# Performance work log

Hardware: AMD Instinct MI355X
Metric: run time of the kernel (lower is better)

The kernel has to match this reference:

```python
import jax, jax.numpy as jnp
import numpy as np

H, C = 5, 12            # heads, head_size
N_NODES, N_EDGES = 100000, 1600000
F_NODE, F_EDGE = 128, 32
HID, N_CLASSES = 16, 2


def _lin_init(key, din, dout, bias=True):
    k1, k2 = jax.random.split(key)
    s = 1.0 / np.sqrt(din)
    W = jax.random.uniform(k1, (din, dout), minval=-s, maxval=s, dtype=jnp.float32)
    if bias:
        b = jax.random.uniform(k2, (dout,), minval=-s, maxval=s, dtype=jnp.float32)
        return W, b
    return W


def setup_inputs() -> dict:
    key = jax.random.key(0)
    ks = jax.random.split(key, 8)
    d = {}
    d["x"] = jax.random.normal(ks[0], (N_NODES, F_NODE), dtype=jnp.float32)
    d["edge_index"] = jax.random.randint(ks[1], (2, N_EDGES), 0, N_NODES)
    d["edge_attr"] = jax.random.normal(ks[2], (N_EDGES, F_EDGE), dtype=jnp.float32)
    HC = H * C
    for i, din in [(1, F_NODE), (2, HC)]:
        kk = jax.random.split(ks[2 + i], 5)
        d[f"Wq{i}"], d[f"bq{i}"] = _lin_init(kk[0], din, HC)
        d[f"Wk{i}"], d[f"bk{i}"] = _lin_init(kk[1], din, HC)
        d[f"Wv{i}"], d[f"bv{i}"] = _lin_init(kk[2], din, HC)
        d[f"We{i}"] = _lin_init(kk[3], F_EDGE, HC, bias=False)  # lin_edge has no bias in PyG
        d[f"Ws{i}"], d[f"bs{i}"] = _lin_init(kk[4], din, HC)    # root/skip linear
    d["W1"], d["b1"] = _lin_init(ks[6], HC, HID)
    d["W2"], d["b2"] = _lin_init(ks[7], HID, N_CLASSES)
    return d


def _transformer_conv(x, src, dst, edge_attr, Wq, bq, Wk, bk, Wv, bv, We, Ws, bs):
    # PyG TransformerConv, concat=True, root_weight=True, beta=False, dropout=0
    N = x.shape[0]
    q = (x @ Wq + bq).reshape(N, H, C)
    k = (x @ Wk + bk).reshape(N, H, C)
    v = (x @ Wv + bv).reshape(N, H, C)
    e = (edge_attr @ We).reshape(-1, H, C)          # [E,H,C]
    kj = k[src] + e                                  # per-edge key
    vj = v[src] + e                                  # per-edge value
    alpha = jnp.einsum('ehc,ehc->eh', q[dst], kj) / jnp.sqrt(jnp.asarray(C, x.dtype))
    # segment-softmax over incoming edges of each destination node
    amax = jax.ops.segment_max(alpha, dst, num_segments=N)          # [N,H]
    w = jnp.exp(alpha - amax[dst])
    denom = jax.ops.segment_sum(w, dst, num_segments=N)             # [N,H]
    w = w / (denom[dst] + 1e-16)
    out = jax.ops.segment_sum(vj * w[:, :, None], dst, num_segments=N).reshape(N, H * C)
    return out + x @ Ws + bs                                         # skip/root connection


def reference(x, edge_index, edge_attr,
              Wq1, bq1, Wk1, bk1, Wv1, bv1, We1, Ws1, bs1,
              Wq2, bq2, Wk2, bk2, Wv2, bv2, We2, Ws2, bs2,
              W1, b1, W2, b2):
    src, dst = edge_index[0], edge_index[1]
    h = jax.nn.relu(_transformer_conv(x, src, dst, edge_attr, Wq1, bq1, Wk1, bk1, Wv1, bv1, We1, Ws1, bs1))
    h = jax.nn.relu(_transformer_conv(h, src, dst, edge_attr, Wq2, bq2, Wk2, bk2, Wv2, bv2, We2, Ws2, bs2))
    h = jax.nn.relu(h @ W1 + b1)
    return h @ W2 + b2
```

## Files before the change

kernel.cpp:

```cpp
#include <hip/hip_runtime.h>
#include <cstddef>

#define NN 100000
#define NE 1600000
#define NH 5
#define NC 12
#define HC 60
#define FN 128
#define FE 32
#define HID 16
#define NCLS 2

template<int DIN>
__global__ __launch_bounds__(256) void qkvs_kernel(
    const float* __restrict__ X,
    const float* __restrict__ Wq, const float* __restrict__ bq,
    const float* __restrict__ Wk, const float* __restrict__ bk,
    const float* __restrict__ Wv, const float* __restrict__ bv,
    const float* __restrict__ Ws, const float* __restrict__ bs,
    float* __restrict__ q, float* __restrict__ k,
    float* __restrict__ v, float* __restrict__ s)
{
    constexpr int NB = 8;
    const int n0 = blockIdx.x * NB;
    const int j = threadIdx.x;
    if (j >= 240) return;
    const int mat = j / 60, col = j - mat * 60;
    const float* W; const float* b; float* out;
    switch (mat) {
        case 0:  W = Wq; b = bq; out = q; break;
        case 1:  W = Wk; b = bk; out = k; break;
        case 2:  W = Wv; b = bv; out = v; break;
        default: W = Ws; b = bs; out = s; break;
    }
    const float* __restrict__ xr = X + (size_t)n0 * DIN;
    float acc[NB];
    #pragma unroll
    for (int m = 0; m < NB; ++m) acc[m] = 0.f;
    #pragma unroll 4
    for (int r = 0; r < DIN; ++r) {
        const float w = W[r * 60 + col];
        #pragma unroll
        for (int m = 0; m < NB; ++m)
            acc[m] = fmaf(xr[(size_t)m * DIN + r], w, acc[m]);
    }
    const float bb = b[col];
    #pragma unroll
    for (int m = 0; m < NB; ++m)
        out[(size_t)(n0 + m) * 60 + col] = acc[m] + bb;
}

__global__ __launch_bounds__(256) void hist_kernel(
    const int* __restrict__ ei, int* __restrict__ cnt)
{
    const int e = blockIdx.x * 256 + threadIdx.x;
    if (e < NE) atomicAdd(&cnt[ei[NE + e]], 1);
}

__global__ __launch_bounds__(1024) void scan1_kernel(
    const int* __restrict__ cnt, int* __restrict__ excl, int* __restrict__ bsum)
{
    __shared__ int sh[1024];
    const int i = blockIdx.x * 1024 + threadIdx.x;
    const int v = (i < NN) ? cnt[i] : 0;
    sh[threadIdx.x] = v;
    __syncthreads();
    for (int off = 1; off < 1024; off <<= 1) {
        const int t = (threadIdx.x >= off) ? sh[threadIdx.x - off] : 0;
        __syncthreads();
        sh[threadIdx.x] += t;
        __syncthreads();
    }
    if (i < NN) excl[i] = sh[threadIdx.x] - v;
    if (threadIdx.x == 1023) bsum[blockIdx.x] = sh[1023];
}

__global__ void scan2_kernel(int* __restrict__ bsum, int nb, int* __restrict__ start)
{
    if (threadIdx.x == 0 && blockIdx.x == 0) {
        int acc = 0;
        for (int b = 0; b < nb; ++b) { const int t = bsum[b]; bsum[b] = acc; acc += t; }
        start[NN] = acc;
    }
}

__global__ __launch_bounds__(1024) void scan3_kernel(
    int* __restrict__ start, const int* __restrict__ bsum)
{
    const int i = blockIdx.x * 1024 + threadIdx.x;
    if (i < NN) start[i] += bsum[blockIdx.x];
}

__global__ __launch_bounds__(256) void scatter_kernel(
    const int* __restrict__ ei, int* __restrict__ cursor,
    int* __restrict__ perm, int* __restrict__ srcs)
{
    const int e = blockIdx.x * 256 + threadIdx.x;
    if (e >= NE) return;
    const int d = ei[NE + e];
    const int pos = atomicAdd(&cursor[d], 1);
    perm[pos] = e;
    srcs[pos] = ei[e];
}

__global__ __launch_bounds__(256) void permea_kernel(
    const int* __restrict__ perm, const float* __restrict__ ea,
    float* __restrict__ eaP)
{
    const int t = blockIdx.x * 256 + threadIdx.x;
    const int slot = t >> 3, r4 = t & 7;
    const int e = perm[slot];
    const float4 val = ((const float4*)(ea + (size_t)e * FE))[r4];
    ((float4*)(eaP + (size_t)slot * FE))[r4] = val;
}

template<bool LIN>
__global__ __launch_bounds__(256) void agg_kernel(
    const int* __restrict__ perm, const int* __restrict__ srcs,
    const int* __restrict__ start,
    const float* __restrict__ ea, const float* __restrict__ We,
    const float* __restrict__ q, const float* __restrict__ k,
    const float* __restrict__ v, const float* __restrict__ sk,
    float* __restrict__ hout)
{
    const int wv    = threadIdx.x >> 6;
    const int lane  = threadIdx.x & 63;
    const int n     = blockIdx.x * 4 + wv;
    const int hc    = (lane < 60) ? lane : 0;
    const int hd    = hc / NC;
    const int hbase = hd * NC;
    const int c     = hc - hbase;

    const int r1 = hbase + ((c + 6) % 12);
    const int r2 = hbase + ((c + 3) % 12);
    const int r3 = hbase + ((c + 1) % 3);
    const int r4 = hbase + ((c + 2) % 3);

    float Wcol[FE];
    #pragma unroll
    for (int r = 0; r < FE; ++r) Wcol[r] = We[r * 60 + hc];

    const float qv = q[(size_t)n * 60 + hc];
    const float sv = sk[(size_t)n * 60 + hc];

    const int s0 = __builtin_amdgcn_readfirstlane(start[n]);
    const int s1 = __builtin_amdgcn_readfirstlane(start[n + 1]);

    float acc = 0.f, den = 0.f;

    auto compute = [&](const float (&EA)[FE], float KV, float VV) {
        float e0 = 0.f, e1 = 0.f;
        #pragma unroll
        for (int r = 0; r < FE; r += 2) {
            e0 = fmaf(EA[r],     Wcol[r],     e0);
            e1 = fmaf(EA[r + 1], Wcol[r + 1], e1);
        }
        const float eacc = e0 + e1;
        const float p  = qv * (KV + eacc);
        const float f1 = p  + __shfl(p,  r1);
        const float f2 = f1 + __shfl(f1, r2);
        const float a  = f2 + __shfl(f2, r3) + __shfl(f2, r4);
        const float w  = __expf(fmaf(a, 0.28867513459481287f, -20.0f));
        acc = fmaf(w, VV + eacc, acc);
        den += w;
    };

    for (int c0 = s0; c0 < s1; c0 += 64) {
        const int cnt = min(64, s1 - c0);

        int myE = 0, myS = 0;
        if (c0 + lane < s1) {
            myS = srcs[c0 + lane];
            if (!LIN) myE = perm[c0 + lane];
        }

        float eaA[FE], eaB[FE];
        float kA = 0.f, vA = 0.f, kB = 0.f, vB = 0.f;
        float kC = 0.f, vC = 0.f, kD = 0.f, vD = 0.f;

        {
            const int sA = __builtin_amdgcn_readlane(myS, 0);
            kA = k[(size_t)sA * 60 + hc];
            vA = v[(size_t)sA * 60 + hc];
            if (cnt > 1) {
                const int sB = __builtin_amdgcn_readlane(myS, 1);
                kB = k[(size_t)sB * 60 + hc];
                vB = v[(size_t)sB * 60 + hc];
            }
            const float* __restrict__ er = LIN
                ? (ea + (size_t)c0 * FE)
                : (ea + (size_t)__builtin_amdgcn_readlane(myE, 0) * FE);
            #pragma unroll
            for (int r = 0; r < FE; ++r) eaA[r] = er[r];
        }

        for (int t = 0; t < cnt; t += 2) {
            if (t + 1 < cnt) {
                const float* __restrict__ er = LIN
                    ? (ea + (size_t)(c0 + t + 1) * FE)
                    : (ea + (size_t)__builtin_amdgcn_readlane(myE, t + 1) * FE);
                #pragma unroll
                for (int r = 0; r < FE; ++r) eaB[r] = er[r];
            }
            if (t + 2 < cnt) {
                const int sC = __builtin_amdgcn_readlane(myS, t + 2);
                kC = k[(size_t)sC * 60 + hc];
                vC = v[(size_t)sC * 60 + hc];
            }
            compute(eaA, kA, vA);
            if (t + 2 < cnt) {
                const float* __restrict__ er = LIN
                    ? (ea + (size_t)(c0 + t + 2) * FE)
                    : (ea + (size_t)__builtin_amdgcn_readlane(myE, t + 2) * FE);
                #pragma unroll
                for (int r = 0; r < FE; ++r) eaA[r] = er[r];
            }
            if (t + 3 < cnt) {
                const int sD = __builtin_amdgcn_readlane(myS, t + 3);
                kD = k[(size_t)sD * 60 + hc];
                vD = v[(size_t)sD * 60 + hc];
            }
            if (t + 1 < cnt) compute(eaB, kB, vB);
            kA = kC; vA = vC; kB = kD; vB = vD;
        }
    }

    if (lane < 60)
        hout[(size_t)n * 60 + hc] = fmaxf(acc / (den + 1e-16f) + sv, 0.f);
}

__global__ __launch_bounds__(256) void mlp_kernel(
    const float* __restrict__ h,
    const float* __restrict__ W1, const float* __restrict__ b1,
    const float* __restrict__ W2, const float* __restrict__ b2,
    float* __restrict__ out)
{
    __shared__ float sW1[60 * HID];
    __shared__ float sb1[HID];
    __shared__ float sW2[HID * NCLS];
    __shared__ float sb2[NCLS];
    for (int i = threadIdx.x; i < 60 * HID; i += 256) sW1[i] = W1[i];
    if (threadIdx.x < HID)        sb1[threadIdx.x] = b1[threadIdx.x];
    if (threadIdx.x < HID * NCLS) sW2[threadIdx.x] = W2[threadIdx.x];
    if (threadIdx.x < NCLS)       sb2[threadIdx.x] = b2[threadIdx.x];
    __syncthreads();

    const int n = blockIdx.x * 256 + threadIdx.x;
    if (n >= NN) return;
    const float* __restrict__ hr = h + (size_t)n * 60;
    float hv[60];
    #pragma unroll
    for (int i = 0; i < 15; ++i) {
        const float4 t = ((const float4*)hr)[i];
        hv[4 * i + 0] = t.x; hv[4 * i + 1] = t.y;
        hv[4 * i + 2] = t.z; hv[4 * i + 3] = t.w;
    }
    float o0 = sb2[0], o1 = sb2[1];
    for (int j = 0; j < HID; ++j) {
        float t = sb1[j];
        #pragma unroll
        for (int i = 0; i < 60; ++i) t = fmaf(hv[i], sW1[i * HID + j], t);
        t = fmaxf(t, 0.f);
        o0 = fmaf(t, sW2[2 * j + 0], o0);
        o1 = fmaf(t, sW2[2 * j + 1], o1);
    }
    out[(size_t)n * 2 + 0] = o0;
    out[(size_t)n * 2 + 1] = o1;
}

extern "C" void kernel_launch(void* const* d_in, const int* in_sizes, int n_in,
                              void* d_out, int out_size, void* d_ws, size_t ws_size,
                              hipStream_t stream)
{
    const float* x   = (const float*)d_in[0];
    const int*   ei  = (const int*)  d_in[1];
    const float* ea  = (const float*)d_in[2];
    const float* Wq1 = (const float*)d_in[3];  const float* bq1 = (const float*)d_in[4];
    const float* Wk1 = (const float*)d_in[5];  const float* bk1 = (const float*)d_in[6];
    const float* Wv1 = (const float*)d_in[7];  const float* bv1 = (const float*)d_in[8];
    const float* We1 = (const float*)d_in[9];
    const float* Ws1 = (const float*)d_in[10]; const float* bs1 = (const float*)d_in[11];
    const float* Wq2 = (const float*)d_in[12]; const float* bq2 = (const float*)d_in[13];
    const float* Wk2 = (const float*)d_in[14]; const float* bk2 = (const float*)d_in[15];
    const float* Wv2 = (const float*)d_in[16]; const float* bv2 = (const float*)d_in[17];
    const float* We2 = (const float*)d_in[18];
    const float* Ws2 = (const float*)d_in[19]; const float* bs2 = (const float*)d_in[20];
    const float* W1  = (const float*)d_in[21]; const float* b1  = (const float*)d_in[22];
    const float* W2  = (const float*)d_in[23]; const float* b2  = (const float*)d_in[24];
    float* out = (float*)d_out;

    int* cnt    = (int*)d_ws;
    int* startp = cnt + NN;
    int* cursor = startp + NN + 1;
    int* bsum   = cursor + NN;
    int* perm   = bsum + 128;
    int* srcs   = perm + NE;
    const size_t int_bytes = (size_t)(3 * NN + 1 + 128 + 2 * NE) * sizeof(int);
    const size_t f_off = (int_bytes + 255) & ~(size_t)255;
    const size_t NHC = (size_t)NN * 60;
    float* qb = (float*)((char*)d_ws + f_off);
    float* kb = qb + NHC;
    float* vb = kb + NHC;
    float* sb = vb + NHC;
    float* h0 = sb + NHC;
    float* eaP = h0 + NHC;
    const size_t need = f_off + 5 * NHC * sizeof(float) + (size_t)NE * FE * sizeof(float);
    const bool lin = ws_size >= need;

    const int qkvs_blocks = NN / 8;
    const int e256_blocks = NE / 256;
    const int scan_blocks = (NN + 1023) / 1024;
    const int agg_blocks  = NN / 4;
    const int mlp_blocks  = (NN + 255) / 256;
    const int perm_blocks = NE * 8 / 256;

    hipMemsetAsync(cnt, 0, (size_t)NN * sizeof(int), stream);
    hist_kernel<<<e256_blocks, 256, 0, stream>>>(ei, cnt);
    scan1_kernel<<<scan_blocks, 1024, 0, stream>>>(cnt, startp, bsum);
    scan2_kernel<<<1, 64, 0, stream>>>(bsum, scan_blocks, startp);
    scan3_kernel<<<scan_blocks, 1024, 0, stream>>>(startp, bsum);
    hipMemcpyAsync(cursor, startp, (size_t)NN * sizeof(int),
                   hipMemcpyDeviceToDevice, stream);
    scatter_kernel<<<e256_blocks, 256, 0, stream>>>(ei, cursor, perm, srcs);
    if (lin)
        permea_kernel<<<perm_blocks, 256, 0, stream>>>(perm, ea, eaP);

    qkvs_kernel<FN><<<qkvs_blocks, 256, 0, stream>>>(
        x, Wq1, bq1, Wk1, bk1, Wv1, bv1, Ws1, bs1, qb, kb, vb, sb);
    if (lin)
        agg_kernel<true><<<agg_blocks, 256, 0, stream>>>(
            perm, srcs, startp, eaP, We1, qb, kb, vb, sb, h0);
    else
        agg_kernel<false><<<agg_blocks, 256, 0, stream>>>(
            perm, srcs, startp, ea, We1, qb, kb, vb, sb, h0);

    qkvs_kernel<HC><<<qkvs_blocks, 256, 0, stream>>>(
        h0, Wq2, bq2, Wk2, bk2, Wv2, bv2, Ws2, bs2, qb, kb, vb, sb);
    if (lin)
        agg_kernel<true><<<agg_blocks, 256, 0, stream>>>(
            perm, srcs, startp, eaP, We2, qb, kb, vb, sb, h0);
    else
        agg_kernel<false><<<agg_blocks, 256, 0, stream>>>(
            perm, srcs, startp, ea, We2, qb, kb, vb, sb, h0);

    mlp_kernel<<<mlp_blocks, 256, 0, stream>>>(h0, W1, b1, W2, b2, out);
}
```

Before: 1.264 ms.

## Fuse edge-attr permutation into scatter, retile QKVS, interleave K/V, streamline aggregation

Several changes land together. The edge-attribute permutation kernel is folded into the scatter kernel, which now copies rows with nontemporal loads and stores. The QKVS projection stages inputs in shared memory and computes 4x4 output tiles with float4 weights, writing K and V interleaved into one buffer. The single-thread block-sum scan becomes a parallel shared-memory scan. The aggregation kernel reads K/V from the interleaved layout, uses ds_bpermute for head reductions and exp2 instead of exp, and drops the per-64-edge chunking in favour of direct per-edge index loads. The goal is fewer launches and less memory traffic; the cost is more code complexity and possibly more register and LDS pressure.

New measurement: 2.295 ms. 1.82x slower.

```diff
diff --git a/kernel.cpp b/kernel.cpp
--- a/kernel.cpp
+++ b/kernel.cpp
@@ -11,6 +11,18 @@
 #define HID 16
 #define NCLS 2
 
+typedef float v4f __attribute__((ext_vector_type(4)));
+
+#if __has_builtin(__builtin_amdgcn_exp2f)
+#define EXP2F(x) __builtin_amdgcn_exp2f(x)
+#else
+#define EXP2F(x) exp2f(x)
+#endif
+
+__device__ __forceinline__ float bperm(int idxb, float x) {
+    return __int_as_float(__builtin_amdgcn_ds_bpermute(idxb, __float_as_int(x)));
+}
+
 template<int DIN>
 __global__ __launch_bounds__(256) void qkvs_kernel(
     const float* __restrict__ X,
@@ -18,36 +30,49 @@
     const float* __restrict__ Wk, const float* __restrict__ bk,
     const float* __restrict__ Wv, const float* __restrict__ bv,
     const float* __restrict__ Ws, const float* __restrict__ bs,
-    float* __restrict__ q, float* __restrict__ k,
-    float* __restrict__ v, float* __restrict__ s)
-{
-    constexpr int NB = 8;
+    float* __restrict__ qb, float* __restrict__ kvb, float* __restrict__ sb)
+{
+    constexpr int NB = 16;
+    __shared__ float xs[NB][DIN + 5];
     const int n0 = blockIdx.x * NB;
-    const int j = threadIdx.x;
-    if (j >= 240) return;
-    const int mat = j / 60, col = j - mat * 60;
-    const float* W; const float* b; float* out;
+    for (int i = threadIdx.x; i < NB * DIN; i += 256) {
+        const int nd = i / DIN, r = i - nd * DIN;
+        xs[nd][r] = X[(size_t)(n0 + nd) * DIN + r];
+    }
+    __syncthreads();
+
+    const int t = threadIdx.x;
+    if (t >= 240) return;
+    const int cg = t % 60, ng = t / 60;
+    const int mat = cg / 15, q4 = (cg % 15) * 4;
+    const float* W; const float* b; float* outp; int ostr;
     switch (mat) {
-        case 0:  W = Wq; b = bq; out = q; break;
-        case 1:  W = Wk; b = bk; out = k; break;
-        case 2:  W = Wv; b = bv; out = v; break;
-        default: W = Ws; b = bs; out = s; break;
-    }
-    const float* __restrict__ xr = X + (size_t)n0 * DIN;
-    float acc[NB];
+        case 0:  W = Wq; b = bq; outp = qb;       ostr = 60;  break;
+        case 1:  W = Wk; b = bk; outp = kvb;      ostr = 120; break;
+        case 2:  W = Wv; b = bv; outp = kvb + 60; ostr = 120; break;
+        default: W = Ws; b = bs; outp = sb;       ostr = 60;  break;
+    }
+    float acc[4][4] = {};
+    #pragma unroll 2
+    for (int r = 0; r < DIN; ++r) {
+        const float4 w = *(const float4*)(W + r * 60 + q4);
+        #pragma unroll
+        for (int j = 0; j < 4; ++j) {
+            const float xv = xs[4 * ng + j][r];
+            acc[j][0] = fmaf(xv, w.x, acc[j][0]);
+            acc[j][1] = fmaf(xv, w.y, acc[j][1]);
+            acc[j][2] = fmaf(xv, w.z, acc[j][2]);
+            acc[j][3] = fmaf(xv, w.w, acc[j][3]);
+        }
+    }
+    const float4 bb = *(const float4*)(b + q4);
     #pragma unroll
-    for (int m = 0; m < NB; ++m) acc[m] = 0.f;
-    #pragma unroll 4
-    for (int r = 0; r < DIN; ++r) {
-        const float w = W[r * 60 + col];
-        #pragma unroll
-        for (int m = 0; m < NB; ++m)
-            acc[m] = fmaf(xr[(size_t)m * DIN + r], w, acc[m]);
-    }
-    const float bb = b[col];
-    #pragma unroll
-    for (int m = 0; m < NB; ++m)
-        out[(size_t)(n0 + m) * 60 + col] = acc[m] + bb;
+    for (int j = 0; j < 4; ++j) {
+        float4 o;
+        o.x = acc[j][0] + bb.x; o.y = acc[j][1] + bb.y;
+        o.z = acc[j][2] + bb.z; o.w = acc[j][3] + bb.w;
+        *(float4*)(outp + (size_t)(n0 + 4 * ng + j) * ostr + q4) = o;
+    }
 }
 
 __global__ __launch_bounds__(256) void hist_kernel(
@@ -75,13 +100,22 @@
     if (threadIdx.x == 1023) bsum[blockIdx.x] = sh[1023];
 }
 
-__global__ void scan2_kernel(int* __restrict__ bsum, int nb, int* __restrict__ start)
-{
-    if (threadIdx.x == 0 && blockIdx.x == 0) {
-        int acc = 0;
-        for (int b = 0; b < nb; ++b) { const int t = bsum[b]; bsum[b] = acc; acc += t; }
-        start[NN] = acc;
-    }
+__global__ __launch_bounds__(128) void scan2_kernel(
+    int* __restrict__ bsum, int nb, int* __restrict__ start)
+{
+    __shared__ int sh[128];
+    const int i = threadIdx.x;
+    const int v = (i < nb) ? bsum[i] : 0;
+    sh[i] = v;
+    __syncthreads();
+    for (int off = 1; off < 128; off <<= 1) {
+        const int tv = (i >= off) ? sh[i - off] : 0;
+        __syncthreads();
+        sh[i] += tv;
+        __syncthreads();
+    }
+    if (i < nb) bsum[i] = sh[i] - v;
+    if (i == 127) start[NN] = sh[127];
 }
 
 __global__ __launch_bounds__(1024) void scan3_kernel(
@@ -93,25 +127,23 @@
 
 __global__ __launch_bounds__(256) void scatter_kernel(
     const int* __restrict__ ei, int* __restrict__ cursor,
-    int* __restrict__ perm, int* __restrict__ srcs)
+    int* __restrict__ perm, int* __restrict__ srcs,
+    const float* __restrict__ ea, float* __restrict__ eaP, const int do_ea)
 {
     const int e = blockIdx.x * 256 + threadIdx.x;
     if (e >= NE) return;
     const int d = ei[NE + e];
     const int pos = atomicAdd(&cursor[d], 1);
-    perm[pos] = e;
     srcs[pos] = ei[e];
-}
-
-__global__ __launch_bounds__(256) void permea_kernel(
-    const int* __restrict__ perm, const float* __restrict__ ea,
-    float* __restrict__ eaP)
-{
-    const int t = blockIdx.x * 256 + threadIdx.x;
-    const int slot = t >> 3, r4 = t & 7;
-    const int e = perm[slot];
-    const float4 val = ((const float4*)(ea + (size_t)e * FE))[r4];
-    ((float4*)(eaP + (size_t)slot * FE))[r4] = val;
+    if (do_ea) {
+        const v4f* s4 = (const v4f*)(ea + (size_t)e * FE);
+        v4f* d4 = (v4f*)(eaP + (size_t)pos * FE);
+        #pragma unroll
+        for (int i = 0; i < 8; ++i)
+            __builtin_nontemporal_store(__builtin_nontemporal_load(s4 + i), d4 + i);
+    } else {
+        perm[pos] = e;
+    }
 }
 
 template<bool LIN>
@@ -119,9 +151,8 @@
     const int* __restrict__ perm, const int* __restrict__ srcs,
     const int* __restrict__ start,
     const float* __restrict__ ea, const float* __restrict__ We,
-    const float* __restrict__ q, const float* __restrict__ k,
-    const float* __restrict__ v, const float* __restrict__ sk,
-    float* __restrict__ hout)
+    const float* __restrict__ q, const float* __restrict__ kv,
+    const float* __restrict__ sk, float* __restrict__ hout)
 {
     const int wv    = threadIdx.x >> 6;
     const int lane  = threadIdx.x & 63;
@@ -131,10 +162,13 @@
     const int hbase = hd * NC;
     const int c     = hc - hbase;
 
-    const int r1 = hbase + ((c + 6) % 12);
-    const int r2 = hbase + ((c + 3) % 12);
-    const int r3 = hbase + ((c + 1) % 3);
-    const int r4 = hbase + ((c + 2) % 3);
+    const int i1 = (hbase + (c + 3) % 12) << 2;
+    const int i2 = (hbase + (c + 6) % 12) << 2;
+    const int i3 = (hbase + (c + 9) % 12) << 2;
+    const int j1 = (hbase + (c + 1) % 3) << 2;
+    const int j2 = (hbase + (c + 2) % 3) << 2;
+
+    const int div0 = (int)__builtin_amdgcn_mbcnt_lo(0u, 0u);
 
     float Wcol[FE];
     #pragma unroll
@@ -148,79 +182,63 @@
 
     float acc = 0.f, den = 0.f;
 
-    auto compute = [&](const float (&EA)[FE], float KV, float VV) {
-        float e0 = 0.f, e1 = 0.f;
-        #pragma unroll
-        for (int r = 0; r < FE; r += 2) {
-            e0 = fmaf(EA[r],     Wcol[r],     e0);
-            e1 = fmaf(EA[r + 1], Wcol[r + 1], e1);
+    auto load_ea = [&](v4f (&E)[8], int tt) {
+        const v4f* er;
+        if (LIN) er = (const v4f*)(ea + (size_t)tt * FE) + div0;
+        else     er = (const v4f*)(ea + (size_t)perm[tt] * FE) + div0;
+        #pragma unroll
+        for (int i = 0; i < 8; ++i) E[i] = __builtin_nontemporal_load(er + i);
+    };
+
+    auto compute = [&](const v4f (&E)[8], float KV, float VV) {
+        float e0 = 0.f, e1 = 0.f, e2 = 0.f, e3 = 0.f;
+        #pragma unroll
+        for (int i = 0; i < 8; ++i) {
+            e0 = fmaf(E[i].x, Wcol[4 * i + 0], e0);
+            e1 = fmaf(E[i].y, Wcol[4 * i + 1], e1);
+            e2 = fmaf(E[i].z, Wcol[4 * i + 2], e2);
+            e3 = fmaf(E[i].w, Wcol[4 * i + 3], e3);
         }
-        const float eacc = e0 + e1;
-        const float p  = qv * (KV + eacc);
-        const float f1 = p  + __shfl(p,  r1);
-        const float f2 = f1 + __shfl(f1, r2);
-        const float a  = f2 + __shfl(f2, r3) + __shfl(f2, r4);
-        const float w  = __expf(fmaf(a, 0.28867513459481287f, -20.0f));
+        const float eacc = (e0 + e1) + (e2 + e3);
+        const float p = qv * (KV + eacc);
+        const float f = (p + bperm(i1, p)) + (bperm(i2, p) + bperm(i3, p));
+        const float a = (f + bperm(j1, f)) + bperm(j2, f);
+        const float w = EXP2F(fmaf(a, 0.41647013f, -28.8539009f));
         acc = fmaf(w, VV + eacc, acc);
         den += w;
     };
 
-    for (int c0 = s0; c0 < s1; c0 += 64) {
-        const int cnt = min(64, s1 - c0);
-
-        int myE = 0, myS = 0;
-        if (c0 + lane < s1) {
-            myS = srcs[c0 + lane];
-            if (!LIN) myE = perm[c0 + lane];
+    v4f eaA[8], eaB[8];
+    float kA = 0.f, vA = 0.f, kB = 0.f, vB = 0.f;
+    float kC = 0.f, vC = 0.f, kD = 0.f, vD = 0.f;
+
+    if (s0 < s1) {
+        {
+            const int sa = srcs[s0];
+            kA = kv[(size_t)sa * 120 + hc];
+            vA = kv[(size_t)sa * 120 + 60 + hc];
+            if (s0 + 1 < s1) {
+                const int sb_ = srcs[s0 + 1];
+                kB = kv[(size_t)sb_ * 120 + hc];
+                vB = kv[(size_t)sb_ * 120 + 60 + hc];
+            }
+            load_ea(eaA, s0);
         }
-
-        float eaA[FE], eaB[FE];
-        float kA = 0.f, vA = 0.f, kB = 0.f, vB = 0.f;
-        float kC = 0.f, vC = 0.f, kD = 0.f, vD = 0.f;
-
-        {
-            const int sA = __builtin_amdgcn_readlane(myS, 0);
-            kA = k[(size_t)sA * 60 + hc];
-            vA = v[(size_t)sA * 60 + hc];
-            if (cnt > 1) {
-                const int sB = __builtin_amdgcn_readlane(myS, 1);
-                kB = k[(size_t)sB * 60 + hc];
-                vB = v[(size_t)sB * 60 + hc];
-            }
-            const float* __restrict__ er = LIN
-                ? (ea + (size_t)c0 * FE)
-                : (ea + (size_t)__builtin_amdgcn_readlane(myE, 0) * FE);
-            #pragma unroll
-            for (int r = 0; r < FE; ++r) eaA[r] = er[r];
-        }
-
-        for (int t = 0; t < cnt; t += 2) {
-            if (t + 1 < cnt) {
-                const float* __restrict__ er = LIN
-                    ? (ea + (size_t)(c0 + t + 1) * FE)
-                    : (ea + (size_t)__builtin_amdgcn_readlane(myE, t + 1) * FE);
-                #pragma unroll
-                for (int r = 0; r < FE; ++r) eaB[r] = er[r];
-            }
-            if (t + 2 < cnt) {
-                const int sC = __builtin_amdgcn_readlane(myS, t + 2);
-                kC = k[(size_t)sC * 60 + hc];
-                vC = v[(size_t)sC * 60 + hc];
+        for (int t = s0; t < s1; t += 2) {
+            if (t + 1 < s1) load_ea(eaB, t + 1);
+            if (t + 2 < s1) {
+                const int sc_ = srcs[t + 2];
+                kC = kv[(size_t)sc_ * 120 + hc];
+                vC = kv[(size_t)sc_ * 120 + 60 + hc];
             }
             compute(eaA, kA, vA);
-            if (t + 2 < cnt) {
-                const float* __restrict__ er = LIN
-                    ? (ea + (size_t)(c0 + t + 2) * FE)
-                    : (ea + (size_t)__builtin_amdgcn_readlane(myE, t + 2) * FE);
-                #pragma unroll
-                for (int r = 0; r < FE; ++r) eaA[r] = er[r];
+            if (t + 2 < s1) load_ea(eaA, t + 2);
+            if (t + 3 < s1) {
+                const int sd_ = srcs[t + 3];
+                kD = kv[(size_t)sd_ * 120 + hc];
+                vD = kv[(size_t)sd_ * 120 + 60 + hc];
             }
-            if (t + 3 < cnt) {
-                const int sD = __builtin_amdgcn_readlane(myS, t + 3);
-                kD = k[(size_t)sD * 60 + hc];
-                vD = v[(size_t)sD * 60 + hc];
-            }
-            if (t + 1 < cnt) compute(eaB, kB, vB);
+            if (t + 1 < s1) compute(eaB, kB, vB);
             kA = kC; vA = vC; kB = kD; vB = vD;
         }
     }
@@ -298,50 +316,47 @@
     const size_t int_bytes = (size_t)(3 * NN + 1 + 128 + 2 * NE) * sizeof(int);
     const size_t f_off = (int_bytes + 255) & ~(size_t)255;
     const size_t NHC = (size_t)NN * 60;
-    float* qb = (float*)((char*)d_ws + f_off);
-    float* kb = qb + NHC;
-    float* vb = kb + NHC;
-    float* sb = vb + NHC;
-    float* h0 = sb + NHC;
+    float* qb  = (float*)((char*)d_ws + f_off);
+    float* kvb = qb + NHC;
+    float* sb  = kvb + 2 * NHC;
+    float* h0  = sb + NHC;
     float* eaP = h0 + NHC;
     const size_t need = f_off + 5 * NHC * sizeof(float) + (size_t)NE * FE * sizeof(float);
     const bool lin = ws_size >= need;
 
-    const int qkvs_blocks = NN / 8;
+    const int qkvs_blocks = NN / 16;
     const int e256_blocks = NE / 256;
     const int scan_blocks = (NN + 1023) / 1024;
     const int agg_blocks  = NN / 4;
     const int mlp_blocks  = (NN + 255) / 256;
-    const int perm_blocks = NE * 8 / 256;
 
     hipMemsetAsync(cnt, 0, (size_t)NN * sizeof(int), stream);
     hist_kernel<<<e256_blocks, 256, 0, stream>>>(ei, cnt);
     scan1_kernel<<<scan_blocks, 1024, 0, stream>>>(cnt, startp, bsum);
-    scan2_kernel<<<1, 64, 0, stream>>>(bsum, scan_blocks, startp);
+    scan2_kernel<<<1, 128, 0, stream>>>(bsum, scan_blocks, startp);
     scan3_kernel<<<scan_blocks, 1024, 0, stream>>>(startp, bsum);
     hipMemcpyAsync(cursor, startp, (size_t)NN * sizeof(int),
                    hipMemcpyDeviceToDevice, stream);
-    scatter_kernel<<<e256_blocks, 256, 0, stream>>>(ei, cursor, perm, srcs);
-    if (lin)
-        permea_kernel<<<perm_blocks, 256, 0, stream>>>(perm, ea, eaP);
+    scatter_kernel<<<e256_blocks, 256, 0, stream>>>(
+        ei, cursor, perm, srcs, ea, eaP, lin ? 1 : 0);
 
     qkvs_kernel<FN><<<qkvs_blocks, 256, 0, stream>>>(
-        x, Wq1, bq1, Wk1, bk1, Wv1, bv1, Ws1, bs1, qb, kb, vb, sb);
+        x, Wq1, bq1, Wk1, bk1, Wv1, bv1, Ws1, bs1, qb, kvb, sb);
     if (lin)
         agg_kernel<true><<<agg_blocks, 256, 0, stream>>>(
-            perm, srcs, startp, eaP, We1, qb, kb, vb, sb, h0);
+            perm, srcs, startp, eaP, We1, qb, kvb, sb, h0);
     else
         agg_kernel<false><<<agg_blocks, 256, 0, stream>>>(
-            perm, srcs, startp, ea, We1, qb, kb, vb, sb, h0);
+            perm, srcs, startp, ea, We1, qb, kvb, sb, h0);
 
     qkvs_kernel<HC><<<qkvs_blocks, 256, 0, stream>>>(
-        h0, Wq2, bq2, Wk2, bk2, Wv2, bv2, Ws2, bs2, qb, kb, vb, sb);
+        h0, Wq2, bq2, Wk2, bk2, Wv2, bv2, Ws2, bs2, qb, kvb, sb);
     if (lin)
         agg_kernel<true><<<agg_blocks, 256, 0, stream>>>(
-            perm, srcs, startp, eaP, We2, qb, kb, vb, sb, h0);
+            perm, srcs, startp, eaP, We2, qb, kvb, sb, h0);
     else
         agg_kernel<false><<<agg_blocks, 256, 0, stream>>>(
-            perm, srcs, startp, ea, We2, qb, kb, vb, sb, h0);
+            perm, srcs, startp, ea, We2, qb, kvb, sb, h0);
 
     mlp_kernel<<<mlp_blocks, 256, 0, stream>>>(h0, W1, b1, W2, b2, out);
 }
```
